# Kernel optimization log

Hardware: AMD Instinct MI355X
Metric: run time of the kernel (lower is better)

The kernel has to match this reference:

```python
import jax, jax.numpy as jnp
import numpy as np
import math

D = 1024
H = 16
DK = D // H
FF = 4096
EPS = 1e-5

def _layer_norm(x, gamma, beta):
    mu = jnp.mean(x, axis=-1, keepdims=True)
    var = jnp.mean((x - mu) ** 2, axis=-1, keepdims=True)
    return (x - mu) * jax.lax.rsqrt(var + EPS) * gamma + beta

def setup_inputs() -> dict:
    key = jax.random.key(0)
    ks = jax.random.split(key, 12)
    B, S = 2, 2048
    s = 1.0 / math.sqrt(D)
    inp = {
        "x": jax.random.normal(ks[0], (B, S, D), jnp.float32),
        "attn_mask": jnp.zeros((B, S, S), jnp.bool_),  # True = masked
        "Wq": jax.random.normal(ks[1], (D, D), jnp.float32) * s,
        "Wk": jax.random.normal(ks[2], (D, D), jnp.float32) * s,
        "Wv": jax.random.normal(ks[3], (D, D), jnp.float32) * s,
        "Wo": jax.random.normal(ks[4], (D, D), jnp.float32) * s,
        "bo": jnp.zeros((D,), jnp.float32),
        "W1": jax.random.normal(ks[5], (D, FF), jnp.float32) * s,
        "b1": jnp.zeros((FF,), jnp.float32),
        "W2": jax.random.normal(ks[6], (FF, D), jnp.float32) * (1.0 / math.sqrt(FF)),
        "b2": jnp.zeros((D,), jnp.float32),
        "g1": jnp.ones((D,), jnp.float32),
        "be1": jnp.zeros((D,), jnp.float32),
        "g2": jnp.ones((D,), jnp.float32),
        "be2": jnp.zeros((D,), jnp.float32),
    }
    return inp

def reference(x, attn_mask, Wq, Wk, Wv, Wo, bo, W1, b1, W2, b2, g1, be1, g2, be2):
    B, S, _ = x.shape
    # QKV projections (no bias), split heads -> [B, H, S, DK]
    q = (x @ Wq).reshape(B, S, H, DK).transpose(0, 2, 1, 3)
    k = (x @ Wk).reshape(B, S, H, DK).transpose(0, 2, 1, 3)
    v = (x @ Wv).reshape(B, S, H, DK).transpose(0, 2, 1, 3)
    scores = jnp.einsum("bhqd,bhkd->bhqk", q, k) / math.sqrt(DK)
    scores = jnp.where(attn_mask[:, None, :, :], -jnp.inf, scores)
    attn = jax.nn.softmax(scores, axis=-1)
    attn = jnp.where(jnp.isnan(attn), 0.0, attn)  # fully-masked-row cleanup
    out = jnp.einsum("bhqk,bhkd->bhqd", attn, v)
    out = out.transpose(0, 2, 1, 3).reshape(B, S, D)
    out = out @ Wo + bo
    # residual + post-LN
    x1 = _layer_norm(out + x, g1, be1)
    # FFN
    f = jax.nn.relu(x1 @ W1 + b1) @ W2 + b2
    return _layer_norm(f + x1, g2, be2)
```

## Files before the change

kernel.cpp:

```cpp
#include <hip/hip_runtime.h>
#include <math.h>

typedef unsigned short u16;
typedef unsigned char u8;
typedef unsigned int u32;
typedef __attribute__((ext_vector_type(4))) float f32x4;
typedef __attribute__((ext_vector_type(8))) short s16x8;
typedef __attribute__((ext_vector_type(4))) short s16x4;
typedef __attribute__((ext_vector_type(4))) u32 u32x4;
typedef __attribute__((ext_vector_type(2))) u32 u32x2;

__device__ __forceinline__ u16 f2bf(float f) {
  unsigned u = __builtin_bit_cast(unsigned, f);
  u += 0x7fffu + ((u >> 16) & 1u);
  return (u16)(u >> 16);
}

__device__ __forceinline__ u32 cvtpk_bf16(float lo, float hi) {
  u32 r;
  asm("v_cvt_pk_bf16_f32 %0, %1, %2" : "=v"(r) : "v"(lo), "v"(hi));
  return r;
}

__device__ __forceinline__ float max3f(float a, float b, float c) {
  return fmaxf(fmaxf(a, b), c);
}

#define GLDS16(g, l) __builtin_amdgcn_global_load_lds( \
    (const __attribute__((address_space(1))) void*)(g), \
    (__attribute__((address_space(3))) void*)(l), 16, 0, 0)

template <int EPI, int BM>
__global__ __launch_bounds__(256, 2) void gemm_bt(
    const u16* __restrict__ A, const u16* __restrict__ BT, int M, int N, int K,
    const float* __restrict__ bias, const float* __restrict__ resid,
    u16* __restrict__ outB, float* __restrict__ outF) {
  constexpr int MT = BM / 32;
  __shared__ __align__(16) u16 lA[2][BM * 32];
  __shared__ __align__(16) u16 lB[2][128 * 32];
  const int tid = threadIdx.x;
  const int wave = __builtin_amdgcn_readfirstlane(tid >> 6);
  const int lane = tid & 63;
  const int l15 = lane & 15, l4 = lane >> 4;
  const int wr = wave >> 1, wc = wave & 1;
  const int row0 = blockIdx.y * BM, col0 = blockIdx.x * 128;

  f32x4 acc[MT][4] = {};

  auto stage = [&](int bi, int k0) {
#pragma unroll
    for (int c = 0; c < BM / 64; ++c) {
      const int chunk = c * 4 + wave;
      const int idx = chunk * 64 + lane;
      const int r = idx >> 2, cb = (idx & 3) * 8;
      GLDS16(A + (size_t)(row0 + r) * K + k0 + cb, &lA[bi][chunk * 512]);
    }
#pragma unroll
    for (int c = 0; c < 2; ++c) {
      const int chunk = c * 4 + wave;
      const int idx = chunk * 64 + lane;
      const int r = idx >> 2, cb = (idx & 3) * 8;
      GLDS16(BT + (size_t)(col0 + r) * K + k0 + cb, &lB[bi][chunk * 512]);
    }
  };

  stage(0, 0);
  __syncthreads();
  int buf = 0;

  for (int k0 = 0; k0 < K; k0 += 32) {
    if (k0 + 32 < K) stage(buf ^ 1, k0 + 32);
    s16x8 af[MT], bfr[4];
#pragma unroll
    for (int m = 0; m < MT; ++m)
      af[m] = *(const s16x8*)&lA[buf][(wr * (BM / 2) + m * 16 + l15) * 32 + l4 * 8];
#pragma unroll
    for (int n = 0; n < 4; ++n)
      bfr[n] = *(const s16x8*)&lB[buf][(wc * 64 + n * 16 + l15) * 32 + l4 * 8];
#pragma unroll
    for (int m = 0; m < MT; ++m)
#pragma unroll
      for (int n = 0; n < 4; ++n)
        acc[m][n] = __builtin_amdgcn_mfma_f32_16x16x32_bf16(af[m], bfr[n], acc[m][n], 0, 0, 0);
    __syncthreads();
    buf ^= 1;
  }

#pragma unroll
  for (int m = 0; m < MT; ++m) {
    const int rowb = row0 + wr * (BM / 2) + m * 16 + l4 * 4;
#pragma unroll
    for (int n = 0; n < 4; ++n) {
      const int col = col0 + wc * 64 + n * 16 + l15;
#pragma unroll
      for (int j = 0; j < 4; ++j) {
        const int r = rowb + j;
        float v = acc[m][n][j];
        if (EPI == 0) {
          outB[(size_t)r * N + col] = f2bf(v);
        } else if (EPI == 1) {
          v += bias[col];
          outB[(size_t)r * N + col] = f2bf(v > 0.0f ? v : 0.0f);
        } else {
          v += bias[col] + resid[(size_t)r * N + col];
          outF[(size_t)r * N + col] = v;
        }
      }
    }
  }
}

__global__ __launch_bounds__(256) void transpose_f32_bf16(
    const float* __restrict__ in, u16* __restrict__ out, int R, int C) {
  __shared__ float t[32][33];
  const int c0 = blockIdx.x * 32, r0 = blockIdx.y * 32;
  const int tx = threadIdx.x & 31, ty = threadIdx.x >> 5;
#pragma unroll
  for (int i = 0; i < 4; ++i)
    t[ty + i * 8][tx] = in[(size_t)(r0 + ty + i * 8) * C + c0 + tx];
  __syncthreads();
#pragma unroll
  for (int i = 0; i < 4; ++i)
    out[(size_t)(c0 + ty + i * 8) * R + r0 + tx] = f2bf(t[tx][ty + i * 8]);
}

__global__ __launch_bounds__(256) void transpose_bf16_b(
    const u16* __restrict__ in, u16* __restrict__ out, int R, int C, int rstr, int coff) {
  __shared__ u16 t[32][34];
  const int b = blockIdx.z;
  const u16* pi = in + (size_t)b * R * rstr + coff;
  u16* po = out + (size_t)b * R * C;
  const int c0 = blockIdx.x * 32, r0 = blockIdx.y * 32;
  const int tx = threadIdx.x & 31, ty = threadIdx.x >> 5;
#pragma unroll
  for (int i = 0; i < 4; ++i)
    t[ty + i * 8][tx] = pi[(size_t)(r0 + ty + i * 8) * rstr + c0 + tx];
  __syncthreads();
#pragma unroll
  for (int i = 0; i < 4; ++i)
    po[(size_t)(c0 + ty + i * 8) * R + r0 + tx] = t[tx][ty + i * 8];
}

__global__ __launch_bounds__(256) void cvt_f32_bf16(
    const float* __restrict__ in, u16* __restrict__ out, int n4) {
  const int i = blockIdx.x * 256 + threadIdx.x;
  if (i >= n4) return;
  f32x4 v = *(const f32x4*)&in[(size_t)i * 4];
  s16x4 o;
#pragma unroll
  for (int j = 0; j < 4; ++j) o[j] = (short)f2bf(v[j]);
  *(s16x4*)&out[(size_t)i * 4] = o;
}

template <int WB>
__global__ __launch_bounds__(256) void layernorm_k(
    const float* __restrict__ in, const float* __restrict__ gm, const float* __restrict__ bt,
    float* __restrict__ outF, u16* __restrict__ outB) {
  const int row = blockIdx.x;
  const int t = threadIdx.x;
  const float* xr = in + (size_t)row * 1024;
  f32x4 v = *(const f32x4*)&xr[t * 4];
  float s = v[0] + v[1] + v[2] + v[3];
  float s2 = v[0] * v[0] + v[1] * v[1] + v[2] * v[2] + v[3] * v[3];
#pragma unroll
  for (int o = 32; o; o >>= 1) {
    s += __shfl_down(s, o);
    s2 += __shfl_down(s2, o);
  }
  __shared__ float red[8];
  const int lane = t & 63, wv = t >> 6;
  if (lane == 0) { red[wv] = s; red[4 + wv] = s2; }
  __syncthreads();
  s = red[0] + red[1] + red[2] + red[3];
  s2 = red[4] + red[5] + red[6] + red[7];
  const float mu = s * (1.0f / 1024.0f);
  const float var = fmaxf(s2 * (1.0f / 1024.0f) - mu * mu, 0.0f);
  const float rs = rsqrtf(var + 1e-5f);
  f32x4 g4 = *(const f32x4*)&gm[t * 4];
  f32x4 b4 = *(const f32x4*)&bt[t * 4];
  f32x4 ov;
#pragma unroll
  for (int j = 0; j < 4; ++j) ov[j] = (v[j] - mu) * rs * g4[j] + b4[j];
  *(f32x4*)&outF[(size_t)row * 1024 + t * 4] = ov;
  if (WB) {
    s16x4 ob;
#pragma unroll
    for (int j = 0; j < 4; ++j) ob[j] = (short)f2bf(ov[j]);
    *(s16x4*)&outB[(size_t)row * 1024 + t * 4] = ob;
  }
}

__global__ __launch_bounds__(256) void mask_summary(
    const u8* __restrict__ mask, u8* __restrict__ msum) {
  const int kt = blockIdx.x, qt = blockIdx.y, b = blockIdx.z;
  const int tid = threadIdx.x;
  __shared__ int any_flag;
  if (tid == 0) any_flag = 0;
  __syncthreads();
  const u8* base = mask + ((size_t)(b * 2048 + qt * 64 + (tid >> 2))) * 2048 + kt * 64 + (tid & 3) * 16;
  const u32x4 v = *(const u32x4*)base;
  if (v[0] | v[1] | v[2] | v[3]) any_flag = 1;
  __syncthreads();
  if (tid == 0) msum[((size_t)b * 32 + qt) * 32 + kt] = (u8)any_flag;
}

__global__ __launch_bounds__(256) void attn_k(
    const u16* __restrict__ QKV, const u16* __restrict__ VT,
    const u8* __restrict__ mask, const u8* __restrict__ msum, u16* __restrict__ out) {
  const int S = 2048, QSTR = 3072, Dm = 1024;
  const int wgid = blockIdx.x + gridDim.x * blockIdx.y;
  const int xcd = wgid & 7, slot = wgid >> 3;
  const int bh = xcd * 4 + (slot >> 5);
  const int qt = slot & 31;
  const int b = bh >> 4, h = bh & 15;
  const int wave = threadIdx.x >> 6, lane = threadIdx.x & 63;
  const int l15 = lane & 15, l4 = lane >> 4;
  const int q0 = qt * 64 + wave * 16;
  const float CE = 0.125f * 1.44269504f;

  __shared__ __align__(16) u16 lK[2][4096];
  __shared__ __align__(16) u16 lV[2][4096];

  const size_t qoff = (size_t)(b * S + q0 + l15) * QSTR + h * 64;
  const s16x8 qa0 = *(const s16x8*)&QKV[qoff + l4 * 8];
  const s16x8 qa1 = *(const s16x8*)&QKV[qoff + 32 + l4 * 8];

  f32x4 o[4] = {};
  float mr = -1e30f, lr = 0.0f;
  const u8* mb = mask + (size_t)b * S * S;
  const u8* msb = msum + (size_t)(b * 32 + qt) * 32;
  const u16* vbase = VT + (size_t)bh * 64 * S;
  const int bS = b * S;

  auto stage = [&](int bi, int kvv) {
#pragma unroll
    for (int c = 0; c < 2; ++c) {
      const int byt = ((c * 4 + wave) * 64 + lane) * 16;
      const int row = byt >> 7;
      const int cb = (byt & 127) ^ ((row & 7) << 4);
      GLDS16(QKV + (size_t)(bS + kvv + row) * QSTR + 1024 + h * 64 + (cb >> 1),
             &lK[bi][(c * 4 + wave) * 512]);
      GLDS16(vbase + (size_t)row * S + kvv + (cb >> 1),
             &lV[bi][(c * 4 + wave) * 512]);
    }
  };

  stage(0, 0);
  __syncthreads();
  int buf = 0;

  for (int kv = 0; kv < S; kv += 64) {
    if (kv + 64 < S) stage(buf ^ 1, kv + 64);
    const char* kbuf = (const char*)&lK[buf][0];
    const char* vbuf = (const char*)&lV[buf][0];

    f32x4 sc[4];
    __builtin_amdgcn_s_setprio(1);
#pragma unroll
    for (int t = 0; t < 4; ++t) {
      const int row = t * 16 + l15;
      const int sw = (row & 7) << 4;
      const s16x8 kf0 = *(const s16x8*)(kbuf + row * 128 + ((l4 * 16) ^ sw));
      const s16x8 kf1 = *(const s16x8*)(kbuf + row * 128 + ((64 + l4 * 16) ^ sw));
      f32x4 z = {};
      z = __builtin_amdgcn_mfma_f32_16x16x32_bf16(kf0, qa0, z, 0, 0, 0);
      z = __builtin_amdgcn_mfma_f32_16x16x32_bf16(kf1, qa1, z, 0, 0, 0);
      sc[t] = z;
    }
    __builtin_amdgcn_s_setprio(0);
    if (msb[kv >> 6]) {
#pragma unroll
      for (int t = 0; t < 4; ++t) {
        const uchar4 m4 = *(const uchar4*)&mb[(size_t)(q0 + l15) * S + kv + t * 16 + l4 * 4];
        if (m4.x) sc[t][0] = -INFINITY;
        if (m4.y) sc[t][1] = -INFINITY;
        if (m4.z) sc[t][2] = -INFINITY;
        if (m4.w) sc[t][3] = -INFINITY;
      }
    }
    float pm = max3f(sc[0][0], sc[0][1], sc[0][2]);
    pm = max3f(pm, sc[0][3], sc[1][0]);
    pm = max3f(pm, sc[1][1], sc[1][2]);
    pm = max3f(pm, sc[1][3], sc[2][0]);
    pm = max3f(pm, sc[2][1], sc[2][2]);
    pm = max3f(pm, sc[2][3], sc[3][0]);
    pm = max3f(pm, sc[3][1], sc[3][2]);
    pm = fmaxf(pm, sc[3][3]);
    pm = fmaxf(pm, __shfl_xor(pm, 16));
    pm = fmaxf(pm, __shfl_xor(pm, 32));
    if (!__all(pm <= mr + 44.0f)) {
      const float mn = fmaxf(mr, pm);
      const float al = exp2f((mr - mn) * CE);
      mr = mn;
      lr *= al;
#pragma unroll
      for (int n = 0; n < 4; ++n)
#pragma unroll
        for (int j = 0; j < 4; ++j) o[n][j] *= al;
    }
    const float mrc = mr * CE;
    float rsum = 0.0f;
#pragma unroll
    for (int t = 0; t < 4; ++t)
#pragma unroll
      for (int j = 0; j < 4; ++j) {
        const float p = exp2f(fmaf(sc[t][j], CE, -mrc));
        sc[t][j] = p;
        rsum += p;
      }
    rsum += __shfl_xor(rsum, 16);
    rsum += __shfl_xor(rsum, 32);
    lr += rsum;
    s16x4 pb[4];
#pragma unroll
    for (int t = 0; t < 4; ++t) {
      const u32 lo = cvtpk_bf16(sc[t][0], sc[t][1]);
      const u32 hi = cvtpk_bf16(sc[t][2], sc[t][3]);
      pb[t] = __builtin_bit_cast(s16x4, u32x2{lo, hi});
    }
    __builtin_amdgcn_s_setprio(1);
#pragma unroll
    for (int n = 0; n < 4; ++n) {
      const int row = n * 16 + l15;
      const int sw = (row & 7) << 4;
#pragma unroll
      for (int t = 0; t < 4; ++t) {
        const s16x4 va = *(const s16x4*)(vbuf + row * 128 + ((t * 32 + l4 * 8) ^ sw));
        o[n] = __builtin_amdgcn_mfma_f32_16x16x16bf16_1k(va, pb[t], o[n], 0, 0, 0);
      }
    }
    __builtin_amdgcn_s_setprio(0);
    __syncthreads();
    buf ^= 1;
  }
  const float inv = lr > 0.0f ? 1.0f / lr : 0.0f;
  const size_t obase = (size_t)(b * S + q0 + l15) * Dm + h * 64;
#pragma unroll
  for (int n = 0; n < 4; ++n) {
    const u32 lo = cvtpk_bf16(o[n][0] * inv, o[n][1] * inv);
    const u32 hi = cvtpk_bf16(o[n][2] * inv, o[n][3] * inv);
    *(u32x2*)&out[obase + n * 16 + l4 * 4] = u32x2{lo, hi};
  }
}

extern "C" void kernel_launch(void* const* d_in, const int* in_sizes, int n_in,
                              void* d_out, int out_size, void* d_ws, size_t ws_size,
                              hipStream_t stream) {
  (void)in_sizes; (void)n_in; (void)out_size; (void)ws_size;
  const float* x = (const float*)d_in[0];
  const u8* mask = (const u8*)d_in[1];
  const float* Wq = (const float*)d_in[2];
  const float* Wk = (const float*)d_in[3];
  const float* Wv = (const float*)d_in[4];
  const float* Wo = (const float*)d_in[5];
  const float* bo = (const float*)d_in[6];
  const float* W1 = (const float*)d_in[7];
  const float* b1 = (const float*)d_in[8];
  const float* W2 = (const float*)d_in[9];
  const float* b2 = (const float*)d_in[10];
  const float* g1 = (const float*)d_in[11];
  const float* be1 = (const float*)d_in[12];
  const float* g2 = (const float*)d_in[13];
  const float* be2 = (const float*)d_in[14];
  float* outp = (float*)d_out;

  const int B = 2, S = 2048, D = 1024, FF = 4096;
  const int M = B * S;
  char* w = (char*)d_ws;
  const size_t MB = 1024 * 1024;
  u16* wqkvT = (u16*)(w + 0 * MB);
  u16* woT = (u16*)(w + 6 * MB);
  u16* w1T = (u16*)(w + 8 * MB);
  u16* w2T = (u16*)(w + 16 * MB);
  u16* xb  = (u16*)(w + 24 * MB);
  u16* qkv = (u16*)(w + 32 * MB);
  u16* vt  = (u16*)(w + 56 * MB);
  float* x0f = (float*)(w + 64 * MB);
  float* x1f = (float*)(w + 80 * MB);
  u16* x1b = (u16*)(w + 96 * MB);
  u8* msum = (u8*)(w + 64 * MB);
  u16* attn_o = xb;
  u16* ff1 = (u16*)(w + 32 * MB);
  float* y0f = x0f;

  transpose_f32_bf16<<<dim3(32, 32), 256, 0, stream>>>(Wq, wqkvT, 1024, 1024);
  transpose_f32_bf16<<<dim3(32, 32), 256, 0, stream>>>(Wk, wqkvT + 1024 * 1024, 1024, 1024);
  transpose_f32_bf16<<<dim3(32, 32), 256, 0, stream>>>(Wv, wqkvT + 2048 * 1024, 1024, 1024);
  transpose_f32_bf16<<<dim3(32, 32), 256, 0, stream>>>(Wo, woT, 1024, 1024);
  transpose_f32_bf16<<<dim3(128, 32), 256, 0, stream>>>(W1, w1T, 1024, 4096);
  transpose_f32_bf16<<<dim3(32, 128), 256, 0, stream>>>(W2, w2T, 4096, 1024);
  cvt_f32_bf16<<<dim3(M * D / 4 / 256), 256, 0, stream>>>(x, xb, M * D / 4);
  mask_summary<<<dim3(32, 32, 2), 256, 0, stream>>>(mask, msum);

  gemm_bt<0, 128><<<dim3(3 * D / 128, M / 128), 256, 0, stream>>>(xb, wqkvT, M, 3 * D, D, nullptr, nullptr, qkv, nullptr);
  transpose_bf16_b<<<dim3(32, 64, 2), 256, 0, stream>>>(qkv, vt, 2048, 1024, 3072, 2048);

  attn_k<<<dim3(32, 32), 256, 0, stream>>>(qkv, vt, mask, msum, attn_o);

  gemm_bt<2, 64><<<dim3(D / 128, M / 64), 256, 0, stream>>>(attn_o, woT, M, D, D, bo, x, nullptr, x0f);
  layernorm_k<1><<<dim3(M), 256, 0, stream>>>(x0f, g1, be1, x1f, x1b);
  gemm_bt<1, 128><<<dim3(FF / 128, M / 128), 256, 0, stream>>>(x1b, w1T, M, FF, D, b1, nullptr, ff1, nullptr);
  gemm_bt<2, 64><<<dim3(D / 128, M / 64), 256, 0, stream>>>(ff1, w2T, M, D, FF, b2, x1f, nullptr, y0f);
  layernorm_k<0><<<dim3(M), 256, 0, stream>>>(y0f, g2, be2, outp, nullptr);
}
```

Baseline: 295.5 us.

## Process two 16-row query groups per wave to reuse K/V LDS fragments

Each attention workgroup now covers 128 query rows (32 per wave, as two 16-row groups), which halves the grid to 512 blocks. K and V fragments are loaded from LDS into registers once per tile and reused for both query groups, cutting LDS read traffic and K/V staging per query. The kv loop is unrolled by two with a fixed buffer index, and masked scores use -1e30 plus a clamp instead of -inf. This raises register pressure and halves the number of workgroups, which could lower occupancy and leave the GPU less full.

```diff
diff --git a/kernel.cpp b/kernel.cpp
--- a/kernel.cpp
+++ b/kernel.cpp
@@ -208,27 +208,31 @@
     const u16* __restrict__ QKV, const u16* __restrict__ VT,
     const u8* __restrict__ mask, const u8* __restrict__ msum, u16* __restrict__ out) {
   const int S = 2048, QSTR = 3072, Dm = 1024;
-  const int wgid = blockIdx.x + gridDim.x * blockIdx.y;
+  const int wgid = blockIdx.x;
   const int xcd = wgid & 7, slot = wgid >> 3;
-  const int bh = xcd * 4 + (slot >> 5);
-  const int qt = slot & 31;
+  const int bh = xcd * 4 + (slot >> 4);
+  const int qt = slot & 15;
   const int b = bh >> 4, h = bh & 15;
   const int wave = threadIdx.x >> 6, lane = threadIdx.x & 63;
   const int l15 = lane & 15, l4 = lane >> 4;
-  const int q0 = qt * 64 + wave * 16;
+  const int q0 = qt * 128 + wave * 32;
   const float CE = 0.125f * 1.44269504f;
 
   __shared__ __align__(16) u16 lK[2][4096];
   __shared__ __align__(16) u16 lV[2][4096];
 
-  const size_t qoff = (size_t)(b * S + q0 + l15) * QSTR + h * 64;
-  const s16x8 qa0 = *(const s16x8*)&QKV[qoff + l4 * 8];
-  const s16x8 qa1 = *(const s16x8*)&QKV[qoff + 32 + l4 * 8];
-
-  f32x4 o[4] = {};
-  float mr = -1e30f, lr = 0.0f;
+  s16x8 qa[2][2];
+#pragma unroll
+  for (int g = 0; g < 2; ++g) {
+    const size_t qoff = (size_t)(b * S + q0 + g * 16 + l15) * QSTR + h * 64;
+    qa[g][0] = *(const s16x8*)&QKV[qoff + l4 * 8];
+    qa[g][1] = *(const s16x8*)&QKV[qoff + 32 + l4 * 8];
+  }
+
+  f32x4 o[2][4] = {};
+  float mr[2] = {-1e30f, -1e30f}, lr[2] = {0.0f, 0.0f};
   const u8* mb = mask + (size_t)b * S * S;
-  const u8* msb = msum + (size_t)(b * 32 + qt) * 32;
+  const u8* msb = msum + (size_t)(b * 32 + qt * 2 + (wave >> 1)) * 32;
   const u16* vbase = VT + (size_t)bh * 64 * S;
   const int bS = b * S;
 
@@ -245,101 +249,121 @@
     }
   };
 
-  stage(0, 0);
-  __syncthreads();
-  int buf = 0;
-
-  for (int kv = 0; kv < S; kv += 64) {
-    if (kv + 64 < S) stage(buf ^ 1, kv + 64);
-    const char* kbuf = (const char*)&lK[buf][0];
-    const char* vbuf = (const char*)&lV[buf][0];
-
-    f32x4 sc[4];
-    __builtin_amdgcn_s_setprio(1);
+  auto body = [&](int bi, int kvv) {
+    if (kvv + 64 < S) stage(bi ^ 1, kvv + 64);
+    const char* kbuf = (const char*)&lK[bi][0];
+    const char* vbuf = (const char*)&lV[bi][0];
+    s16x8 kf[4][2];
 #pragma unroll
     for (int t = 0; t < 4; ++t) {
       const int row = t * 16 + l15;
       const int sw = (row & 7) << 4;
-      const s16x8 kf0 = *(const s16x8*)(kbuf + row * 128 + ((l4 * 16) ^ sw));
-      const s16x8 kf1 = *(const s16x8*)(kbuf + row * 128 + ((64 + l4 * 16) ^ sw));
-      f32x4 z = {};
-      z = __builtin_amdgcn_mfma_f32_16x16x32_bf16(kf0, qa0, z, 0, 0, 0);
-      z = __builtin_amdgcn_mfma_f32_16x16x32_bf16(kf1, qa1, z, 0, 0, 0);
-      sc[t] = z;
-    }
-    __builtin_amdgcn_s_setprio(0);
-    if (msb[kv >> 6]) {
-#pragma unroll
-      for (int t = 0; t < 4; ++t) {
-        const uchar4 m4 = *(const uchar4*)&mb[(size_t)(q0 + l15) * S + kv + t * 16 + l4 * 4];
-        if (m4.x) sc[t][0] = -INFINITY;
-        if (m4.y) sc[t][1] = -INFINITY;
-        if (m4.z) sc[t][2] = -INFINITY;
-        if (m4.w) sc[t][3] = -INFINITY;
-      }
-    }
-    float pm = max3f(sc[0][0], sc[0][1], sc[0][2]);
-    pm = max3f(pm, sc[0][3], sc[1][0]);
-    pm = max3f(pm, sc[1][1], sc[1][2]);
-    pm = max3f(pm, sc[1][3], sc[2][0]);
-    pm = max3f(pm, sc[2][1], sc[2][2]);
-    pm = max3f(pm, sc[2][3], sc[3][0]);
-    pm = max3f(pm, sc[3][1], sc[3][2]);
-    pm = fmaxf(pm, sc[3][3]);
-    pm = fmaxf(pm, __shfl_xor(pm, 16));
-    pm = fmaxf(pm, __shfl_xor(pm, 32));
-    if (!__all(pm <= mr + 44.0f)) {
-      const float mn = fmaxf(mr, pm);
-      const float al = exp2f((mr - mn) * CE);
-      mr = mn;
-      lr *= al;
-#pragma unroll
-      for (int n = 0; n < 4; ++n)
-#pragma unroll
-        for (int j = 0; j < 4; ++j) o[n][j] *= al;
-    }
-    const float mrc = mr * CE;
-    float rsum = 0.0f;
-#pragma unroll
-    for (int t = 0; t < 4; ++t)
-#pragma unroll
-      for (int j = 0; j < 4; ++j) {
-        const float p = exp2f(fmaf(sc[t][j], CE, -mrc));
-        sc[t][j] = p;
-        rsum += p;
-      }
-    rsum += __shfl_xor(rsum, 16);
-    rsum += __shfl_xor(rsum, 32);
-    lr += rsum;
-    s16x4 pb[4];
-#pragma unroll
-    for (int t = 0; t < 4; ++t) {
-      const u32 lo = cvtpk_bf16(sc[t][0], sc[t][1]);
-      const u32 hi = cvtpk_bf16(sc[t][2], sc[t][3]);
-      pb[t] = __builtin_bit_cast(s16x4, u32x2{lo, hi});
-    }
-    __builtin_amdgcn_s_setprio(1);
+      kf[t][0] = *(const s16x8*)(kbuf + row * 128 + ((l4 * 16) ^ sw));
+      kf[t][1] = *(const s16x8*)(kbuf + row * 128 + ((64 + l4 * 16) ^ sw));
+    }
+    s16x4 va[4][4];
 #pragma unroll
     for (int n = 0; n < 4; ++n) {
       const int row = n * 16 + l15;
       const int sw = (row & 7) << 4;
 #pragma unroll
+      for (int t = 0; t < 4; ++t)
+        va[n][t] = *(const s16x4*)(vbuf + row * 128 + ((t * 32 + l4 * 8) ^ sw));
+    }
+    const int mrow = msb[kvv >> 6];
+#pragma unroll
+    for (int g = 0; g < 2; ++g) {
+      f32x4 sc[4];
+      __builtin_amdgcn_s_setprio(1);
+#pragma unroll
       for (int t = 0; t < 4; ++t) {
-        const s16x4 va = *(const s16x4*)(vbuf + row * 128 + ((t * 32 + l4 * 8) ^ sw));
-        o[n] = __builtin_amdgcn_mfma_f32_16x16x16bf16_1k(va, pb[t], o[n], 0, 0, 0);
+        f32x4 z = {};
+        z = __builtin_amdgcn_mfma_f32_16x16x32_bf16(kf[t][0], qa[g][0], z, 0, 0, 0);
+        z = __builtin_amdgcn_mfma_f32_16x16x32_bf16(kf[t][1], qa[g][1], z, 0, 0, 0);
+        sc[t] = z;
       }
-    }
-    __builtin_amdgcn_s_setprio(0);
+      __builtin_amdgcn_s_setprio(0);
+      if (mrow) {
+#pragma unroll
+        for (int t = 0; t < 4; ++t) {
+          const uchar4 m4 = *(const uchar4*)&mb[(size_t)(q0 + g * 16 + l15) * S + kvv + t * 16 + l4 * 4];
+          if (m4.x) sc[t][0] = -1e30f;
+          if (m4.y) sc[t][1] = -1e30f;
+          if (m4.z) sc[t][2] = -1e30f;
+          if (m4.w) sc[t][3] = -1e30f;
+        }
+      }
+#pragma unroll
+      for (int t = 0; t < 4; ++t)
+#pragma unroll
+        for (int j = 0; j < 4; ++j) sc[t][j] = fminf(sc[t][j], 1e30f);
+      float pm = max3f(sc[0][0], sc[0][1], sc[0][2]);
+      pm = max3f(pm, sc[0][3], sc[1][0]);
+      pm = max3f(pm, sc[1][1], sc[1][2]);
+      pm = max3f(pm, sc[1][3], sc[2][0]);
+      pm = max3f(pm, sc[2][1], sc[2][2]);
+      pm = max3f(pm, sc[2][3], sc[3][0]);
+      pm = max3f(pm, sc[3][1], sc[3][2]);
+      pm = fmaxf(pm, sc[3][3]);
+      pm = fmaxf(pm, __shfl_xor(pm, 16));
+      pm = fmaxf(pm, __shfl_xor(pm, 32));
+      if (!__all(pm <= mr[g] + 44.0f)) {
+        const float mn = fmaxf(mr[g], pm);
+        const float al = exp2f((mr[g] - mn) * CE);
+        mr[g] = mn;
+        lr[g] *= al;
+#pragma unroll
+        for (int n = 0; n < 4; ++n)
+#pragma unroll
+          for (int j = 0; j < 4; ++j) o[g][n][j] *= al;
+      }
+      const float mrc = mr[g] * CE;
+      float rsum = 0.0f;
+#pragma unroll
+      for (int t = 0; t < 4; ++t)
+#pragma unroll
+        for (int j = 0; j < 4; ++j) {
+          const float p = exp2f(fmaf(sc[t][j], CE, -mrc));
+          sc[t][j] = p;
+          rsum += p;
+        }
+      rsum += __shfl_xor(rsum, 16);
+      rsum += __shfl_xor(rsum, 32);
+      lr[g] += rsum;
+      s16x4 pb[4];
+#pragma unroll
+      for (int t = 0; t < 4; ++t) {
+        const u32 lo = cvtpk_bf16(sc[t][0], sc[t][1]);
+        const u32 hi = cvtpk_bf16(sc[t][2], sc[t][3]);
+        pb[t] = __builtin_bit_cast(s16x4, u32x2{lo, hi});
+      }
+      __builtin_amdgcn_s_setprio(1);
+#pragma unroll
+      for (int n = 0; n < 4; ++n)
+#pragma unroll
+        for (int t = 0; t < 4; ++t)
+          o[g][n] = __builtin_amdgcn_mfma_f32_16x16x16bf16_1k(va[n][t], pb[t], o[g][n], 0, 0, 0);
+      __builtin_amdgcn_s_setprio(0);
+    }
     __syncthreads();
-    buf ^= 1;
-  }
-  const float inv = lr > 0.0f ? 1.0f / lr : 0.0f;
-  const size_t obase = (size_t)(b * S + q0 + l15) * Dm + h * 64;
-#pragma unroll
-  for (int n = 0; n < 4; ++n) {
-    const u32 lo = cvtpk_bf16(o[n][0] * inv, o[n][1] * inv);
-    const u32 hi = cvtpk_bf16(o[n][2] * inv, o[n][3] * inv);
-    *(u32x2*)&out[obase + n * 16 + l4 * 4] = u32x2{lo, hi};
+  };
+
+  stage(0, 0);
+  __syncthreads();
+  for (int kv = 0; kv < S; kv += 128) {
+    body(0, kv);
+    body(1, kv + 64);
+  }
+#pragma unroll
+  for (int g = 0; g < 2; ++g) {
+    const float inv = lr[g] > 0.0f ? 1.0f / lr[g] : 0.0f;
+    const size_t obase = (size_t)(b * S + q0 + g * 16 + l15) * Dm + h * 64;
+#pragma unroll
+    for (int n = 0; n < 4; ++n) {
+      const u32 lo = cvtpk_bf16(o[g][n][0] * inv, o[g][n][1] * inv);
+      const u32 hi = cvtpk_bf16(o[g][n][2] * inv, o[g][n][3] * inv);
+      *(u32x2*)&out[obase + n * 16 + l4 * 4] = u32x2{lo, hi};
+    }
   }
 }
 
@@ -395,7 +419,7 @@
   gemm_bt<0, 128><<<dim3(3 * D / 128, M / 128), 256, 0, stream>>>(xb, wqkvT, M, 3 * D, D, nullptr, nullptr, qkv, nullptr);
   transpose_bf16_b<<<dim3(32, 64, 2), 256, 0, stream>>>(qkv, vt, 2048, 1024, 3072, 2048);
 
-  attn_k<<<dim3(32, 32), 256, 0, stream>>>(qkv, vt, mask, msum, attn_o);
+  attn_k<<<dim3(512), 256, 0, stream>>>(qkv, vt, mask, msum, attn_o);
 
   gemm_bt<2, 64><<<dim3(D / 128, M / 64), 256, 0, stream>>>(attn_o, woT, M, D, D, bo, x, nullptr, x0f);
   layernorm_k<1><<<dim3(M), 256, 0, stream>>>(x0f, g1, be1, x1f, x1b);
```

Result: slower. 303.2 us (+2.6%).

## Split attention KV range across two workgroups, add combine kernel, remap GEMM tiles per XCD

Applied to the files above, without the earlier changes.

The attention kernel now splits each (batch, head, query-tile) across two workgroups, each covering half of the KV sequence. This doubles the grid to give more parallelism and occupancy. Each half writes fp32 partial outputs plus its running max and sum, and a new combine kernel merges them with a log-sum-exp rescale and writes the bf16 output. Masked scores are set to a large finite negative value and scores are clamped so the partial merge stays finite. The KV loop is unrolled by two so buffer indices are constants. Separately, the GEMM remaps workgroup IDs so consecutive tiles land on the same XCD for better L2 reuse. The split adds 32MB of fp32 partial traffic and one extra kernel launch.

```diff
diff --git a/kernel.cpp b/kernel.cpp
--- a/kernel.cpp
+++ b/kernel.cpp
@@ -43,7 +43,11 @@
   const int lane = tid & 63;
   const int l15 = lane & 15, l4 = lane >> 4;
   const int wr = wave >> 1, wc = wave & 1;
-  const int row0 = blockIdx.y * BM, col0 = blockIdx.x * 128;
+  const int nwg = gridDim.x * gridDim.y;
+  int wg = blockIdx.y * gridDim.x + blockIdx.x;
+  wg = (wg & 7) * (nwg >> 3) + (wg >> 3);
+  const int bx = wg % gridDim.x, by = wg / gridDim.x;
+  const int row0 = by * BM, col0 = bx * 128;
 
   f32x4 acc[MT][4] = {};
 
@@ -206,16 +210,20 @@
 
 __global__ __launch_bounds__(256) void attn_k(
     const u16* __restrict__ QKV, const u16* __restrict__ VT,
-    const u8* __restrict__ mask, const u8* __restrict__ msum, u16* __restrict__ out) {
-  const int S = 2048, QSTR = 3072, Dm = 1024;
-  const int wgid = blockIdx.x + gridDim.x * blockIdx.y;
+    const u8* __restrict__ mask, const u8* __restrict__ msum,
+    float* __restrict__ opart, float* __restrict__ mlpart) {
+  const int S = 2048, QSTR = 3072;
+  const int wgid = blockIdx.x;
   const int xcd = wgid & 7, slot = wgid >> 3;
-  const int bh = xcd * 4 + (slot >> 5);
-  const int qt = slot & 31;
+  const int bh = xcd * 4 + (slot >> 6);
+  const int rem = slot & 63;
+  const int kvh = rem >> 5;
+  const int qt = rem & 31;
   const int b = bh >> 4, h = bh & 15;
   const int wave = threadIdx.x >> 6, lane = threadIdx.x & 63;
   const int l15 = lane & 15, l4 = lane >> 4;
   const int q0 = qt * 64 + wave * 16;
+  const int kv0 = kvh * 1024, kvend = kv0 + 1024;
   const float CE = 0.125f * 1.44269504f;
 
   __shared__ __align__(16) u16 lK[2][4096];
@@ -245,14 +253,10 @@
     }
   };
 
-  stage(0, 0);
-  __syncthreads();
-  int buf = 0;
-
-  for (int kv = 0; kv < S; kv += 64) {
-    if (kv + 64 < S) stage(buf ^ 1, kv + 64);
-    const char* kbuf = (const char*)&lK[buf][0];
-    const char* vbuf = (const char*)&lV[buf][0];
+  auto body = [&](int bi, int kvv) {
+    if (kvv + 64 < kvend) stage(bi ^ 1, kvv + 64);
+    const char* kbuf = (const char*)&lK[bi][0];
+    const char* vbuf = (const char*)&lV[bi][0];
 
     f32x4 sc[4];
     __builtin_amdgcn_s_setprio(1);
@@ -268,16 +272,20 @@
       sc[t] = z;
     }
     __builtin_amdgcn_s_setprio(0);
-    if (msb[kv >> 6]) {
+    if (msb[kvv >> 6]) {
 #pragma unroll
       for (int t = 0; t < 4; ++t) {
-        const uchar4 m4 = *(const uchar4*)&mb[(size_t)(q0 + l15) * S + kv + t * 16 + l4 * 4];
-        if (m4.x) sc[t][0] = -INFINITY;
-        if (m4.y) sc[t][1] = -INFINITY;
-        if (m4.z) sc[t][2] = -INFINITY;
-        if (m4.w) sc[t][3] = -INFINITY;
+        const uchar4 m4 = *(const uchar4*)&mb[(size_t)(q0 + l15) * S + kvv + t * 16 + l4 * 4];
+        if (m4.x) sc[t][0] = -1e30f;
+        if (m4.y) sc[t][1] = -1e30f;
+        if (m4.z) sc[t][2] = -1e30f;
+        if (m4.w) sc[t][3] = -1e30f;
       }
     }
+#pragma unroll
+    for (int t = 0; t < 4; ++t)
+#pragma unroll
+      for (int j = 0; j < 4; ++j) sc[t][j] = fminf(sc[t][j], 1e30f);
     float pm = max3f(sc[0][0], sc[0][1], sc[0][2]);
     pm = max3f(pm, sc[0][3], sc[1][0]);
     pm = max3f(pm, sc[1][1], sc[1][2]);
@@ -331,16 +339,44 @@
     }
     __builtin_amdgcn_s_setprio(0);
     __syncthreads();
-    buf ^= 1;
-  }
-  const float inv = lr > 0.0f ? 1.0f / lr : 0.0f;
-  const size_t obase = (size_t)(b * S + q0 + l15) * Dm + h * 64;
-#pragma unroll
-  for (int n = 0; n < 4; ++n) {
-    const u32 lo = cvtpk_bf16(o[n][0] * inv, o[n][1] * inv);
-    const u32 hi = cvtpk_bf16(o[n][2] * inv, o[n][3] * inv);
-    *(u32x2*)&out[obase + n * 16 + l4 * 4] = u32x2{lo, hi};
-  }
+  };
+
+  stage(0, kv0);
+  __syncthreads();
+  for (int kv = kv0; kv < kvend; kv += 128) {
+    body(0, kv);
+    body(1, kv + 64);
+  }
+  const int prow = q0 + l15;
+  float* obase = opart + ((size_t)kvh * 65536 + (size_t)bh * 2048 + prow) * 64;
+#pragma unroll
+  for (int n = 0; n < 4; ++n)
+    *(f32x4*)&obase[n * 16 + l4 * 4] = o[n];
+  if (l4 == 0) {
+    const size_t mli = ((size_t)kvh * 65536 + (size_t)bh * 2048 + prow) * 2;
+    mlpart[mli] = mr;
+    mlpart[mli + 1] = lr;
+  }
+}
+
+__global__ __launch_bounds__(256) void attn_combine(
+    const float* __restrict__ opart, const float* __restrict__ mlpart,
+    u16* __restrict__ out) {
+  const int row = blockIdx.x * 4 + (threadIdx.x >> 6);
+  const int lane = threadIdx.x & 63;
+  const float CE = 0.125f * 1.44269504f;
+  const float m1 = mlpart[(size_t)row * 2], l1 = mlpart[(size_t)row * 2 + 1];
+  const float m2 = mlpart[65536ull * 2 + (size_t)row * 2], l2 = mlpart[65536ull * 2 + (size_t)row * 2 + 1];
+  const float m = fmaxf(m1, m2);
+  const float a1 = exp2f((m1 - m) * CE);
+  const float a2 = exp2f((m2 - m) * CE);
+  const float l = a1 * l1 + a2 * l2;
+  const float inv = l > 0.0f ? 1.0f / l : 0.0f;
+  const float o1 = opart[(size_t)row * 64 + lane];
+  const float o2 = opart[65536ull * 64 + (size_t)row * 64 + lane];
+  const float ov = (a1 * o1 + a2 * o2) * inv;
+  const int bh = row >> 11, q = row & 2047;
+  out[((size_t)((bh >> 4) * 2048 + q)) * 1024 + (bh & 15) * 64 + lane] = f2bf(ov);
 }
 
 extern "C" void kernel_launch(void* const* d_in, const int* in_sizes, int n_in,
@@ -379,6 +415,8 @@
   float* x1f = (float*)(w + 80 * MB);
   u16* x1b = (u16*)(w + 96 * MB);
   u8* msum = (u8*)(w + 64 * MB);
+  float* opart = (float*)(w + 65 * MB);
+  float* mlpart = (float*)(w + 99 * MB);
   u16* attn_o = xb;
   u16* ff1 = (u16*)(w + 32 * MB);
   float* y0f = x0f;
@@ -395,7 +433,8 @@
   gemm_bt<0, 128><<<dim3(3 * D / 128, M / 128), 256, 0, stream>>>(xb, wqkvT, M, 3 * D, D, nullptr, nullptr, qkv, nullptr);
   transpose_bf16_b<<<dim3(32, 64, 2), 256, 0, stream>>>(qkv, vt, 2048, 1024, 3072, 2048);
 
-  attn_k<<<dim3(32, 32), 256, 0, stream>>>(qkv, vt, mask, msum, attn_o);
+  attn_k<<<dim3(2048), 256, 0, stream>>>(qkv, vt, mask, msum, opart, mlpart);
+  attn_combine<<<dim3(65536 / 4), 256, 0, stream>>>(opart, mlpart, attn_o);
 
   gemm_bt<2, 64><<<dim3(D / 128, M / 64), 256, 0, stream>>>(attn_o, woT, M, D, D, bo, x, nullptr, x0f);
   layernorm_k<1><<<dim3(M), 256, 0, stream>>>(x0f, g1, be1, x1f, x1b);
```

Measured after the change: 301.5 us. +2.0%, slower.
